# Kernel optimization log

Hardware: AMD Instinct MI355X
Metric: run time of the kernel (lower is better)

Reference implementation:

```python
import jax, jax.numpy as jnp
import numpy as np

B, N = 4, 1024
D1, D2 = 512, 512
C = 512          # out_c = outdim_self[2] = ln_dim
H = 8            # cross_num_heads
DH = C // H      # head dim
LAYERS = 3       # cross_layer
LN_EPS = 1e-5


def _layer_norm(x, gamma, beta):
    mu = jnp.mean(x, axis=-1, keepdims=True)
    var = jnp.mean(jnp.square(x - mu), axis=-1, keepdims=True)
    return (x - mu) * jax.lax.rsqrt(var + LN_EPS) * gamma + beta


def setup_inputs() -> dict:
    key = jax.random.key(0)
    ks = jax.random.split(key, 5)
    s1, s2, sv = 1.0 / np.sqrt(D1), 1.0 / np.sqrt(D2), 1.0 / np.sqrt(D1 + D2)
    return {
        "x1": jax.random.normal(ks[0], (B, N, D1), jnp.float32),
        "x2": jax.random.normal(ks[1], (B, N, D2), jnp.float32),
        "Wq": jax.random.uniform(ks[2], (C, D1), jnp.float32, -s1, s1),
        "Wk": jax.random.uniform(ks[3], (C, D2), jnp.float32, -s2, s2),
        "Wv": jax.random.uniform(ks[4], (C, D1 + D2), jnp.float32, -sv, sv),
        "ln_gamma": jnp.ones((C,), jnp.float32),
        "ln_beta": jnp.zeros((C,), jnp.float32),
    }


def reference(x1, x2, Wq, Wk, Wv, ln_gamma, ln_beta):
    x = jnp.concatenate((x1, x2), axis=2)                      # [B,N,D1+D2]
    scale = x1.shape[-1] ** (-0.5)                             # uses x1 feature dim
    # [B,N,C] -> [B,H,N,DH]
    to_heads = lambda t: t.reshape(B, N, H, DH).transpose(0, 2, 1, 3)
    Q = to_heads(jnp.einsum('bnd,cd->bnc', x1, Wq))
    K = to_heads(jnp.einsum('bnd,cd->bnc', x2, Wk))
    V = to_heads(jnp.einsum('bnd,cd->bnc', x, Wv))

    output = None
    for _ in range(LAYERS):
        attn = jnp.einsum('bhnd,bhmd->bhnm', Q, K) * scale     # [B,H,N,N]
        mask = attn != 0
        attn = jnp.where(mask, attn, -1e20)
        attn = jax.nn.softmax(attn, axis=-1)
        attn = attn * mask
        V1 = jnp.einsum('bhnm,bhmd->bhnd', attn, V)            # [B,H,N,DH]
        V1 = V1.transpose(0, 2, 1, 3).reshape(B, N, C)
        Vr = V.transpose(0, 2, 1, 3).reshape(B, N, C)
        output = _layer_norm(V1 + Vr, ln_gamma, ln_beta)       # [B,N,C]
        V = to_heads(output)
    return output
```

## Files before the change

### kernel.cpp

```cpp
#include <hip/hip_runtime.h>


#define LOG2E 1.44269504088896f

using f32x4   = __attribute__((ext_vector_type(4))) float;
using short8  = __attribute__((ext_vector_type(8))) short;
using ushort8 = __attribute__((ext_vector_type(8))) unsigned short;
using uchar8  = __attribute__((ext_vector_type(8))) unsigned char;
using uchar16 = __attribute__((ext_vector_type(16))) unsigned char;

__device__ inline unsigned short f2bf(float f) {
  unsigned u = __builtin_bit_cast(unsigned, f);
  u += 0x7fffu + ((u >> 16) & 1u);
  return (unsigned short)(u >> 16);
}
__device__ inline float bf2f(unsigned short h) {
  unsigned u = (unsigned)h << 16;
  return __builtin_bit_cast(float, u);
}

__device__ inline unsigned char f2e4m3_fast(float f) {
  unsigned u = __builtin_bit_cast(unsigned, f);
  unsigned sign = (u >> 24) & 0x80u;
  unsigned a = u & 0x7fffffffu;
  unsigned v = a + (0x7ffffu + ((a >> 20) & 1u));
  unsigned m = (v >> 20) - 960u;
  m = (m > 126u) ? 126u : m;
  m = (a < 0x3c000000u) ? 0u : m;
  return (unsigned char)(sign | m);
}

__device__ inline f32x4 mfma_bf16(short8 a, short8 b, f32x4 c) {
  return __builtin_amdgcn_mfma_f32_16x16x32_bf16(a, b, c, 0, 0, 0);
}

__device__ inline void gload_lds16(const void* g, void* l) {
  __builtin_amdgcn_global_load_lds(
      (const __attribute__((address_space(1))) unsigned int*)g,
      (__attribute__((address_space(3))) unsigned int*)l, 16, 0, 0);
}

__device__ inline int swz(int row, int byte_in_row) {
  return row * 128 + (byte_in_row ^ ((row & 7) << 4));
}

__global__ __launch_bounds__(256) void k_convert_all(
    const float* __restrict__ x1, const float* __restrict__ x2,
    const float* __restrict__ Wq, const float* __restrict__ Wk,
    const float* __restrict__ Wv,
    unsigned short* __restrict__ xb, unsigned short* __restrict__ Wqb,
    unsigned short* __restrict__ Wkb, unsigned short* __restrict__ Wvb) {
  int i = blockIdx.x * 256 + threadIdx.x;
  const float* src;
  unsigned short* dst;
  if (i < 524288) {
    int e0 = i * 8, m = e0 >> 10, d = e0 & 1023;
    src = (d < 512) ? (x1 + (size_t)m * 512 + d)
                    : (x2 + (size_t)m * 512 + (d - 512));
    dst = xb + (size_t)e0;
  } else if (i < 557056) {
    int j = (i - 524288) * 8;
    src = Wq + j; dst = Wqb + j;
  } else if (i < 589824) {
    int j = (i - 557056) * 8;
    src = Wk + j; dst = Wkb + j;
  } else {
    int j = (i - 589824) * 8;
    src = Wv + j; dst = Wvb + j;
  }
  float4 a = ((const float4*)src)[0];
  float4 b = ((const float4*)src)[1];
  ushort8 o;
  o[0] = f2bf(a.x); o[1] = f2bf(a.y); o[2] = f2bf(a.z); o[3] = f2bf(a.w);
  o[4] = f2bf(b.x); o[5] = f2bf(b.y); o[6] = f2bf(b.z); o[7] = f2bf(b.w);
  *(ushort8*)dst = o;
}

__global__ __launch_bounds__(256) void k_proj(
    const unsigned short* __restrict__ xb,
    const unsigned short* __restrict__ Wqb,
    const unsigned short* __restrict__ Wkb,
    const unsigned short* __restrict__ Wvb,
    unsigned short* __restrict__ Qb, unsigned short* __restrict__ Kb,
    float* __restrict__ Vf) {
  __shared__ __align__(16) unsigned short Atile[128 * 64];
  __shared__ __align__(16) unsigned short Btile[128 * 64];

  const int id  = blockIdx.x;
  const int z   = id % 3;
  const int rem = id / 3;
  const int c0  = (rem & 3) * 128;
  const int m0  = (rem >> 2) * 128;

  const int K    = (z == 2) ? 1024 : 512;
  const int aoff = (z == 1) ? 512 : 0;
  const unsigned short* W = (z == 0) ? Wqb : (z == 1) ? Wkb : Wvb;

  const int t  = threadIdx.x;
  const int w  = t >> 6, l = t & 63;
  const int lr = l & 15, ls = l >> 4;
  const int wr = w >> 1, wc = w & 1;

  const int srow  = l >> 3;
  const int scol8 = (l & 7) * 8;

  f32x4 acc[4][4] = {};

  for (int k0 = 0; k0 < K; k0 += 64) {
#pragma unroll
    for (int j = 0; j < 4; ++j) {
      int ch  = w * 4 + j;
      int row = ch * 8 + srow;
      gload_lds16(xb + (size_t)(m0 + row) * 1024 + aoff + k0 + scol8,
                  Atile + ch * 512);
      gload_lds16(W + (size_t)(c0 + row) * K + k0 + scol8,
                  Btile + ch * 512);
    }
    __syncthreads();
#pragma unroll
    for (int ks = 0; ks < 2; ++ks) {
      short8 af[4], bf[4];
#pragma unroll
      for (int mf = 0; mf < 4; ++mf)
        af[mf] = *(const short8*)(Atile + (wr * 64 + mf * 16 + lr) * 64 +
                                  ks * 32 + ls * 8);
#pragma unroll
      for (int nf = 0; nf < 4; ++nf)
        bf[nf] = *(const short8*)(Btile + (wc * 64 + nf * 16 + lr) * 64 +
                                  ks * 32 + ls * 8);
#pragma unroll
      for (int mf = 0; mf < 4; ++mf)
#pragma unroll
        for (int nf = 0; nf < 4; ++nf)
          acc[mf][nf] = mfma_bf16(af[mf], bf[nf], acc[mf][nf]);
    }
    __syncthreads();
  }

#pragma unroll
  for (int mf = 0; mf < 4; ++mf)
#pragma unroll
    for (int nf = 0; nf < 4; ++nf)
#pragma unroll
      for (int r = 0; r < 4; ++r) {
        int m = m0 + wr * 64 + mf * 16 + ls * 4 + r;
        int c = c0 + wc * 64 + nf * 16 + lr;
        float v = acc[mf][nf][r];
        if (z == 2) {
          Vf[(size_t)m * 512 + c] = v;
        } else {
          int b = m >> 10, n = m & 1023, h = c >> 6, dh = c & 63;
          size_t idx = ((size_t)(b * 8 + h) * 1024 + n) * 64 + dh;
          (z == 0 ? Qb : Kb)[idx] = f2bf(v);
        }
      }
}

__global__ __launch_bounds__(256) void k_transpose_v(
    const float* __restrict__ Vf, void* __restrict__ Vt, int mode) {
  __shared__ unsigned short tile[64 * 66];
  const int bh = blockIdx.y;
  const int b = bh >> 3, h = bh & 7;
  const int n0 = blockIdx.x * 64;
  const int t = threadIdx.x;
  {
    int n = t >> 2, dh0 = (t & 3) * 16;
    const float* src = Vf + ((size_t)b * 1024 + n0 + n) * 512 + h * 64 + dh0;
    unsigned short* dst = tile + n * 66 + dh0;
#pragma unroll
    for (int j = 0; j < 16; j += 4) {
      float4 v = *(const float4*)(src + j);
      dst[j + 0] = f2bf(v.x); dst[j + 1] = f2bf(v.y);
      dst[j + 2] = f2bf(v.z); dst[j + 3] = f2bf(v.w);
    }
  }
  __syncthreads();
#pragma unroll
  for (int it = 0; it < 2; ++it) {
    int dh = (t >> 3) + it * 32, n8 = (t & 7) * 8;
    if (mode == 0) {
      ushort8 o;
#pragma unroll
      for (int j = 0; j < 8; ++j) o[j] = tile[(n8 + j) * 66 + dh];
      char* dst = (char*)Vt + ((size_t)(bh * 64 + dh)) * 2048 + n0 * 2 +
                  ((n8 * 2) ^ ((dh & 7) << 4));
      *(ushort8*)dst = o;
    } else {
      uchar8 o;
#pragma unroll
      for (int j = 0; j < 8; ++j)
        o[j] = f2e4m3_fast(bf2f(tile[(n8 + j) * 66 + dh]));
      int byte = n0 + n8;
      char* dst = (char*)Vt + ((size_t)(bh * 64 + dh)) * 1024 + (byte & ~127) +
                  ((byte & 127) ^ ((dh & 7) << 4));
      *(uchar8*)dst = o;
    }
  }
}

__global__ __launch_bounds__(256) void k_scores(
    const unsigned short* __restrict__ Qb,
    const unsigned short* __restrict__ Kb,
    unsigned char* __restrict__ Pmat, float* __restrict__ lsum_g) {
  __shared__ char lds[8192 + 4 * 16 * 80];
  char* kbuf = lds;
  const int id  = blockIdx.x;
  const int lid = (id & 7) * 128 + (id >> 3);
  const int bh  = lid >> 5;
  const int q0  = ((lid >> 1) & 15) * 64;
  const int kh  = lid & 1;
  const int t = threadIdx.x;
  const int w = t >> 6, l = t & 63, lr = l & 15, ls = l >> 4;
  char* pbuf = lds + 8192 + w * (16 * 80);

  const float sclog2e = 0.0637587160f;

  short8 qa[2];
  {
    const unsigned short* Qg =
        Qb + ((size_t)bh * 1024 + q0 + w * 16 + lr) * 64 + ls * 8;
    qa[0] = *(const short8*)(Qg);
    qa[1] = *(const short8*)(Qg + 32);
  }

  const unsigned short* Kg = Kb + (size_t)bh * 1024 * 64 + kh * 512 * 64;
  unsigned char* Pg = Pmat + (size_t)bh * 1024 * 1024;

  float lacc[4] = {0.f, 0.f, 0.f, 0.f};

  const int srow = t >> 3, sc8 = (t & 7) * 8;
  int4 kreg[2];
  kreg[0] = *(const int4*)(Kg + (size_t)(srow)*64 + sc8);
  kreg[1] = *(const int4*)(Kg + (size_t)(srow + 32) * 64 + sc8);

  for (int kc = 0; kc < 8; ++kc) {
    *(int4*)(kbuf + swz(srow, sc8 * 2)) = kreg[0];
    *(int4*)(kbuf + swz(srow + 32, sc8 * 2)) = kreg[1];
    __syncthreads();
    if (kc < 7) {
      kreg[0] = *(const int4*)(Kg + (size_t)((kc + 1) * 64 + srow) * 64 + sc8);
      kreg[1] = *(const int4*)(Kg + (size_t)((kc + 1) * 64 + srow + 32) * 64 + sc8);
    }

    f32x4 s[4] = {};
#pragma unroll
    for (int kk = 0; kk < 2; ++kk) {
#pragma unroll
      for (int nt = 0; nt < 4; ++nt) {
        short8 bk = *(const short8*)(kbuf + swz(nt * 16 + lr, kk * 64 + ls * 16));
        s[nt] = mfma_bf16(qa[kk], bk, s[nt]);
      }
    }

#pragma unroll
    for (int nt = 0; nt < 4; ++nt)
#pragma unroll
      for (int r = 0; r < 4; ++r) {
        float sv = s[nt][r];
        float pv = (sv == 0.f) ? 0.f : __builtin_amdgcn_exp2f(sv * sclog2e);
        lacc[r] += pv;
        pbuf[(ls * 4 + r) * 80 + nt * 16 + lr] = (char)f2e4m3_fast(pv);
      }

    int gkc = kh * 8 + kc;
    {
      int prow = l >> 2, pchk = l & 3;
      uchar16 pv16 = *(const uchar16*)(pbuf + prow * 80 + pchk * 16);
      int n = q0 + w * 16 + prow;
      *(uchar16*)(Pg + (size_t)n * 1024 + (gkc >> 1) * 128 +
                  (((gkc & 1) * 64 + pchk * 16) ^ ((n & 7) << 4))) = pv16;
    }
    __syncthreads();
  }

#pragma unroll
  for (int r = 0; r < 4; ++r) {
#pragma unroll
    for (int off = 1; off < 16; off <<= 1)
      lacc[r] += __shfl_xor(lacc[r], off, 64);
  }
  if (lr == 0) {
#pragma unroll
    for (int r = 0; r < 4; ++r)
      lsum_g[kh * 32768 + (size_t)bh * 1024 + q0 + w * 16 + ls * 4 + r] =
          lacc[r];
  }
}

__global__ __launch_bounds__(256) void k_pv(
    const unsigned char* __restrict__ Pmat,
    const unsigned char* __restrict__ Vt,
    const float* __restrict__ lsum_g, float* __restrict__ V1a,
    float* __restrict__ V1b) {
  __shared__ __align__(16) char Ab[2][8192];
  __shared__ __align__(16) char Bb[2][8192];
  const int id  = blockIdx.x;
  const int lid = (id & 7) * 128 + (id >> 3);
  const int head = lid >> 5;
  const int n0   = ((lid >> 1) & 15) * 64;
  const int mh   = lid & 1;
  const int t = threadIdx.x;
  const int w = t >> 6, l = t & 63, lr = l & 15, ls = l >> 4;

  const char* Pg = (const char*)(Pmat + (size_t)head * 1024 * 1024) +
                   (size_t)n0 * 1024 + mh * 512;
  const char* Vg = (const char*)(Vt + (size_t)head * 64 * 1024) + mh * 512;

  const int srow = w * 16 + (l >> 3);
  const int sc16 = (l & 7) * 16;

  f32x4 acc[4] = {};

  auto STAGE = [&](int buf, int kc) {
#pragma unroll
    for (int j = 0; j < 2; ++j) {
      int row = srow + j * 8;
      gload_lds16(Pg + (size_t)row * 1024 + kc * 128 + sc16,
                  &Ab[buf][w * 2048 + j * 1024]);
      gload_lds16(Vg + (size_t)row * 1024 + kc * 128 + sc16,
                  &Bb[buf][w * 2048 + j * 1024]);
    }
  };

  STAGE(0, 0);
  __syncthreads();
  int cur = 0;
  for (int kc = 0; kc < 4; ++kc) {
    if (kc < 3) STAGE(cur ^ 1, kc + 1);
#pragma unroll
    for (int ks = 0; ks < 4; ++ks) {
      long af = *(const long*)(&Ab[cur][swz(w * 16 + lr, ks * 32 + ls * 8)]);
#pragma unroll
      for (int nf = 0; nf < 4; ++nf) {
        long bf8 = *(const long*)(&Bb[cur][swz(nf * 16 + lr, ks * 32 + ls * 8)]);
        acc[nf] = __builtin_amdgcn_mfma_f32_16x16x32_fp8_fp8(af, bf8, acc[nf],
                                                             0, 0, 0);
      }
    }
    __syncthreads();
    cur ^= 1;
  }

  float* V1 = mh ? V1b : V1a;
  const int b = head >> 3, h = head & 7;
#pragma unroll
  for (int r = 0; r < 4; ++r) {
    int n = n0 + w * 16 + ls * 4 + r;
    float lv = lsum_g[(size_t)head * 1024 + n] +
               lsum_g[32768 + (size_t)head * 1024 + n];
    float rinv = (lv > 0.f) ? 1.f / lv : 0.f;
#pragma unroll
    for (int nf = 0; nf < 4; ++nf)
      V1[((size_t)b * 1024 + n) * 512 + h * 64 + nf * 16 + lr] =
          acc[nf][r] * rinv;
  }
}

__global__ __launch_bounds__(256) void k_ln_t(
    const float* __restrict__ V1a, const float* __restrict__ V1b,
    const float* __restrict__ Vf_in,
    const float* __restrict__ gamma, const float* __restrict__ beta,
    float* __restrict__ Vf_out, void* __restrict__ Vt, int mode) {
  __shared__ unsigned short tile[16 * 520];
  const int blk = blockIdx.x;
  const int b  = blk >> 6;
  const int n0 = (blk & 63) * 16;
  const int t = threadIdx.x;
  const int row = t >> 4;
  const int c0  = (t & 15) * 32;
  const size_t base = ((size_t)b * 1024 + n0 + row) * 512 + c0;

  float x[32];
  float s = 0.f, sq = 0.f;
#pragma unroll
  for (int j = 0; j < 32; j += 4) {
    float4 a0 = *(const float4*)(V1a + base + j);
    float4 a1 = *(const float4*)(V1b + base + j);
    float4 v = *(const float4*)(Vf_in + base + j);
    float4 y = {a0.x + a1.x + v.x, a0.y + a1.y + v.y, a0.z + a1.z + v.z,
                a0.w + a1.w + v.w};
    x[j + 0] = y.x; x[j + 1] = y.y; x[j + 2] = y.z; x[j + 3] = y.w;
    s  += y.x + y.y + y.z + y.w;
    sq += y.x * y.x + y.y * y.y + y.z * y.z + y.w * y.w;
  }
#pragma unroll
  for (int off = 1; off < 16; off <<= 1) {
    s  += __shfl_xor(s, off, 64);
    sq += __shfl_xor(sq, off, 64);
  }
  float mu   = s * (1.f / 512.f);
  float var  = sq * (1.f / 512.f) - mu * mu;
  float rstd = rsqrtf(var + 1e-5f);

  unsigned short* trow = tile + row * 520 + c0;
#pragma unroll
  for (int j = 0; j < 32; j += 4) {
    float4 g = *(const float4*)(gamma + c0 + j);
    float4 bb = *(const float4*)(beta + c0 + j);
    float4 y;
    y.x = (x[j + 0] - mu) * rstd * g.x + bb.x;
    y.y = (x[j + 1] - mu) * rstd * g.y + bb.y;
    y.z = (x[j + 2] - mu) * rstd * g.z + bb.z;
    y.w = (x[j + 3] - mu) * rstd * g.w + bb.w;
    *(float4*)(Vf_out + base + j) = y;
    if (mode != 2) {
      trow[j + 0] = f2bf(y.x); trow[j + 1] = f2bf(y.y);
      trow[j + 2] = f2bf(y.z); trow[j + 3] = f2bf(y.w);
    }
  }
  if (mode == 2) return;
  __syncthreads();

#pragma unroll
  for (int it = 0; it < 2; ++it) {
    int d = t + it * 256;
    int h = d >> 6, dh = d & 63;
    int sw = (dh & 7) << 4;
    if (mode == 0) {
      ushort8 o0, o1;
#pragma unroll
      for (int j = 0; j < 8; ++j) {
        o0[j] = tile[j * 520 + d];
        o1[j] = tile[(j + 8) * 520 + d];
      }
      int byte0 = n0 * 2;
      char* rowb = (char*)Vt + ((size_t)((b * 8 + h) * 64 + dh)) * 2048 +
                   (byte0 & ~127);
      *(ushort8*)(rowb + ((byte0 & 127) ^ sw)) = o0;
      *(ushort8*)(rowb + (((byte0 & 127) + 16) ^ sw)) = o1;
    } else {
      uchar16 o;
#pragma unroll
      for (int j = 0; j < 16; ++j) o[j] = f2e4m3_fast(bf2f(tile[j * 520 + d]));
      char* rowb = (char*)Vt + ((size_t)((b * 8 + h) * 64 + dh)) * 1024 +
                   (n0 & ~127);
      *(uchar16*)(rowb + ((n0 & 127) ^ sw)) = o;
    }
  }
}

__global__ __launch_bounds__(256) void k_attn(
    const unsigned short* __restrict__ Qb,
    const unsigned short* __restrict__ Kb,
    const unsigned short* __restrict__ Vt,
    float* __restrict__ V1) {
  __shared__ char lds[8192 + 8192 + 4 * 16 * 144];
  char* kbuf = lds;
  char* vbuf = lds + 8192;
  const int bh = blockIdx.y;
  const int q0 = blockIdx.x * 64;
  const int t = threadIdx.x;
  const int w = t >> 6, l = t & 63, lr = l & 15, ls = l >> 4;
  char* pbuf = lds + 16384 + w * (16 * 144);

  const float scale = 0.044194173824159216f;

  short8 qa[2];
  {
    const unsigned short* Qg =
        Qb + ((size_t)bh * 1024 + q0 + w * 16 + lr) * 64 + ls * 8;
    qa[0] = *(const short8*)(Qg);
    qa[1] = *(const short8*)(Qg + 32);
  }

  f32x4 O[4] = {};
  float mrow[4], lrow[4];
#pragma unroll
  for (int r = 0; r < 4; ++r) { mrow[r] = -INFINITY; lrow[r] = 0.f; }

  const unsigned short* Kg = Kb + (size_t)bh * 1024 * 64;
  const char* Vg = (const char*)(Vt + (size_t)bh * 64 * 1024);

  for (int kc = 0; kc < 16; ++kc) {
    {
      int row = t >> 3;
      int c8  = (t & 7) * 8;
#pragma unroll
      for (int it = 0; it < 2; ++it) {
        int rr = row + it * 32;
        int4 kv = *(const int4*)(Kg + (size_t)(kc * 64 + rr) * 64 + c8);
        *(int4*)(kbuf + swz(rr, c8 * 2)) = kv;
        int swv = (rr & 7) << 4;
        int4 vv = *(const int4*)(Vg + (size_t)rr * 2048 + kc * 128 +
                                 ((c8 * 2) ^ swv));
        *(int4*)(vbuf + swz(rr, c8 * 2)) = vv;
      }
    }
    __syncthreads();

    f32x4 s[4] = {};
#pragma unroll
    for (int kk = 0; kk < 2; ++kk) {
#pragma unroll
      for (int nt = 0; nt < 4; ++nt) {
        short8 bk = *(const short8*)(kbuf + swz(nt * 16 + lr, kk * 64 + ls * 16));
        s[nt] = mfma_bf16(qa[kk], bk, s[nt]);
      }
    }

    float p[4][4];
    float cmax[4];
#pragma unroll
    for (int r = 0; r < 4; ++r) cmax[r] = -INFINITY;
#pragma unroll
    for (int nt = 0; nt < 4; ++nt)
#pragma unroll
      for (int r = 0; r < 4; ++r) {
        float sv = s[nt][r];
        p[nt][r] = (sv == 0.f) ? -INFINITY : sv * scale;
        cmax[r] = fmaxf(cmax[r], p[nt][r]);
      }
#pragma unroll
    for (int r = 0; r < 4; ++r)
#pragma unroll
      for (int off = 1; off < 16; off <<= 1)
        cmax[r] = fmaxf(cmax[r], __shfl_xor(cmax[r], off, 64));

    float alpha[4];
#pragma unroll
    for (int r = 0; r < 4; ++r) {
      float mnew = fmaxf(mrow[r], cmax[r]);
      alpha[r] = (mnew == -INFINITY) ? 1.f : exp2f((mrow[r] - mnew) * LOG2E);
      mrow[r] = mnew;
    }
    float lsum[4] = {0.f, 0.f, 0.f, 0.f};
#pragma unroll
    for (int nt = 0; nt < 4; ++nt)
#pragma unroll
      for (int r = 0; r < 4; ++r) {
        float pv = (p[nt][r] == -INFINITY)
                       ? 0.f
                       : exp2f((p[nt][r] - mrow[r]) * LOG2E);
        p[nt][r] = pv;
        lsum[r] += pv;
      }
#pragma unroll
    for (int r = 0; r < 4; ++r) {
#pragma unroll
      for (int off = 1; off < 16; off <<= 1)
        lsum[r] += __shfl_xor(lsum[r], off, 64);
      lrow[r] = lrow[r] * alpha[r] + lsum[r];
    }
#pragma unroll
    for (int dt = 0; dt < 4; ++dt)
#pragma unroll
      for (int r = 0; r < 4; ++r) O[dt][r] *= alpha[r];

#pragma unroll
    for (int nt = 0; nt < 4; ++nt)
#pragma unroll
      for (int r = 0; r < 4; ++r)
        *(unsigned short*)(pbuf + (ls * 4 + r) * 144 + (nt * 16 + lr) * 2) =
            f2bf(p[nt][r]);

#pragma unroll
    for (int kk = 0; kk < 2; ++kk) {
      short8 pa = *(const short8*)(pbuf + lr * 144 + kk * 64 + ls * 16);
#pragma unroll
      for (int dt = 0; dt < 4; ++dt) {
        short8 bv = *(const short8*)(vbuf + swz(dt * 16 + lr, kk * 64 + ls * 16));
        O[dt] = mfma_bf16(pa, bv, O[dt]);
      }
    }
    __syncthreads();
  }

  float rinv[4];
#pragma unroll
  for (int r = 0; r < 4; ++r) rinv[r] = (lrow[r] > 0.f) ? 1.f / lrow[r] : 0.f;
  const int b = bh >> 3, h = bh & 7;
#pragma unroll
  for (int dt = 0; dt < 4; ++dt)
#pragma unroll
    for (int r = 0; r < 4; ++r) {
      int n = q0 + w * 16 + ls * 4 + r;
      int c = h * 64 + dt * 16 + lr;
      V1[((size_t)b * 1024 + n) * 512 + c] = O[dt][r] * rinv[r];
    }
}

extern "C" void kernel_launch(void* const* d_in, const int* in_sizes, int n_in,
                              void* d_out, int out_size, void* d_ws,
                              size_t ws_size, hipStream_t stream) {
  const float* x1    = (const float*)d_in[0];
  const float* x2    = (const float*)d_in[1];
  const float* Wq    = (const float*)d_in[2];
  const float* Wk    = (const float*)d_in[3];
  const float* Wv    = (const float*)d_in[4];
  const float* gamma = (const float*)d_in[5];
  const float* beta  = (const float*)d_in[6];
  float* out = (float*)d_out;
  char* ws = (char*)d_ws;

  const size_t MB = 1u << 20;
  unsigned short* xb  = (unsigned short*)(ws);
  unsigned short* Wqb = (unsigned short*)(ws + 8 * MB);
  unsigned short* Wkb = (unsigned short*)(ws + 8 * MB + 512 * 1024);
  unsigned short* Wvb = (unsigned short*)(ws + 9 * MB);
  unsigned short* Qb  = (unsigned short*)(ws + 10 * MB);
  unsigned short* Kb  = (unsigned short*)(ws + 14 * MB);
  void*           Vt  = (void*)(ws + 18 * MB);
  float*          Vf  = (float*)(ws + 22 * MB);
  float*          V1a = (float*)(ws + 30 * MB);
  float*          lsm = (float*)(ws + 38 * MB);
  unsigned char*  Pm  = (unsigned char*)(ws + 39 * MB);
  float*          V1b = (float*)(ws);

  const bool bigws = ws_size >= (size_t)71 * MB;

  k_convert_all<<<2560, 256, 0, stream>>>(x1, x2, Wq, Wk, Wv, xb, Wqb, Wkb,
                                          Wvb);
  k_proj<<<384, 256, 0, stream>>>(xb, Wqb, Wkb, Wvb, Qb, Kb, Vf);

  if (bigws) {
    k_transpose_v<<<dim3(16, 32), 256, 0, stream>>>(Vf, Vt, 1);
    k_scores<<<1024, 256, 0, stream>>>(Qb, Kb, Pm, lsm);
    for (int layer = 0; layer < 3; ++layer) {
      k_pv<<<1024, 256, 0, stream>>>(Pm, (const unsigned char*)Vt, lsm, V1a,
                                     V1b);
      if (layer < 2)
        k_ln_t<<<256, 256, 0, stream>>>(V1a, V1b, Vf, gamma, beta, Vf, Vt, 1);
      else
        k_ln_t<<<256, 256, 0, stream>>>(V1a, V1b, Vf, gamma, beta, out, Vt, 2);
    }
  } else {
    hipMemsetAsync(V1b, 0, 8 * MB, stream);
    k_transpose_v<<<dim3(16, 32), 256, 0, stream>>>(Vf, Vt, 0);
    for (int layer = 0; layer < 3; ++layer) {
      k_attn<<<dim3(16, 32), 256, 0, stream>>>(Qb, Kb,
                                               (const unsigned short*)Vt, V1a);
      if (layer < 2)
        k_ln_t<<<256, 256, 0, stream>>>(V1a, V1b, Vf, gamma, beta, Vf, Vt, 0);
      else
        k_ln_t<<<256, 256, 0, stream>>>(V1a, V1b, Vf, gamma, beta, out, Vt, 2);
    }
  }
}
```

Baseline: 136.2 us.

## Split score kernel into key quarters with double-buffered K, finer LN blocks

k_scores now splits each query tile's keys into four quarters instead of two, doubling the grid, and double-buffers the K tile in LDS so that one barrier per iteration suffices. The row-sum partials grow to four slices, which k_pv now adds together. k_ln_t processes 4 rows per block instead of 16, with one wavefront per row, giving 1024 blocks. The aim is more parallelism and fewer barriers on the MI355X CUs, at the cost of smaller, narrower global stores (4-byte Vt writes) and extra lsum reads.

```diff
diff --git a/kernel.cpp b/kernel.cpp
--- a/kernel.cpp
+++ b/kernel.cpp
@@ -6,7 +6,9 @@
 using f32x4   = __attribute__((ext_vector_type(4))) float;
 using short8  = __attribute__((ext_vector_type(8))) short;
 using ushort8 = __attribute__((ext_vector_type(8))) unsigned short;
+using ushort4v= __attribute__((ext_vector_type(4))) unsigned short;
 using uchar8  = __attribute__((ext_vector_type(8))) unsigned char;
+using uchar4v = __attribute__((ext_vector_type(4))) unsigned char;
 using uchar16 = __attribute__((ext_vector_type(16))) unsigned char;
 
 __device__ inline unsigned short f2bf(float f) {
@@ -202,16 +204,17 @@
     const unsigned short* __restrict__ Qb,
     const unsigned short* __restrict__ Kb,
     unsigned char* __restrict__ Pmat, float* __restrict__ lsum_g) {
-  __shared__ char lds[8192 + 4 * 16 * 80];
-  char* kbuf = lds;
+  __shared__ char lds[2 * 8192 + 4 * 16 * 80];
+  char* kbuf0 = lds;
+  char* kbuf1 = lds + 8192;
   const int id  = blockIdx.x;
-  const int lid = (id & 7) * 128 + (id >> 3);
-  const int bh  = lid >> 5;
-  const int q0  = ((lid >> 1) & 15) * 64;
-  const int kh  = lid & 1;
+  const int lid = (id & 7) * 256 + (id >> 3);
+  const int bh  = lid >> 6;
+  const int q0  = ((lid >> 2) & 15) * 64;
+  const int kq  = lid & 3;
   const int t = threadIdx.x;
   const int w = t >> 6, l = t & 63, lr = l & 15, ls = l >> 4;
-  char* pbuf = lds + 8192 + w * (16 * 80);
+  char* pbuf = lds + 16384 + w * (16 * 80);
 
   const float sclog2e = 0.0637587160f;
 
@@ -223,7 +226,7 @@
     qa[1] = *(const short8*)(Qg + 32);
   }
 
-  const unsigned short* Kg = Kb + (size_t)bh * 1024 * 64 + kh * 512 * 64;
+  const unsigned short* Kg = Kb + (size_t)bh * 1024 * 64 + kq * 256 * 64;
   unsigned char* Pg = Pmat + (size_t)bh * 1024 * 1024;
 
   float lacc[4] = {0.f, 0.f, 0.f, 0.f};
@@ -232,12 +235,17 @@
   int4 kreg[2];
   kreg[0] = *(const int4*)(Kg + (size_t)(srow)*64 + sc8);
   kreg[1] = *(const int4*)(Kg + (size_t)(srow + 32) * 64 + sc8);
-
-  for (int kc = 0; kc < 8; ++kc) {
-    *(int4*)(kbuf + swz(srow, sc8 * 2)) = kreg[0];
-    *(int4*)(kbuf + swz(srow + 32, sc8 * 2)) = kreg[1];
+  {
+    char* kb = kbuf0;
+    *(int4*)(kb + swz(srow, sc8 * 2)) = kreg[0];
+    *(int4*)(kb + swz(srow + 32, sc8 * 2)) = kreg[1];
+  }
+
+  for (int kc = 0; kc < 4; ++kc) {
     __syncthreads();
-    if (kc < 7) {
+    char* kb  = (kc & 1) ? kbuf1 : kbuf0;
+    char* kbn = (kc & 1) ? kbuf0 : kbuf1;
+    if (kc < 3) {
       kreg[0] = *(const int4*)(Kg + (size_t)((kc + 1) * 64 + srow) * 64 + sc8);
       kreg[1] = *(const int4*)(Kg + (size_t)((kc + 1) * 64 + srow + 32) * 64 + sc8);
     }
@@ -247,7 +255,7 @@
     for (int kk = 0; kk < 2; ++kk) {
 #pragma unroll
       for (int nt = 0; nt < 4; ++nt) {
-        short8 bk = *(const short8*)(kbuf + swz(nt * 16 + lr, kk * 64 + ls * 16));
+        short8 bk = *(const short8*)(kb + swz(nt * 16 + lr, kk * 64 + ls * 16));
         s[nt] = mfma_bf16(qa[kk], bk, s[nt]);
       }
     }
@@ -262,7 +270,7 @@
         pbuf[(ls * 4 + r) * 80 + nt * 16 + lr] = (char)f2e4m3_fast(pv);
       }
 
-    int gkc = kh * 8 + kc;
+    int gkc = kq * 4 + kc;
     {
       int prow = l >> 2, pchk = l & 3;
       uchar16 pv16 = *(const uchar16*)(pbuf + prow * 80 + pchk * 16);
@@ -270,7 +278,11 @@
       *(uchar16*)(Pg + (size_t)n * 1024 + (gkc >> 1) * 128 +
                   (((gkc & 1) * 64 + pchk * 16) ^ ((n & 7) << 4))) = pv16;
     }
-    __syncthreads();
+
+    if (kc < 3) {
+      *(int4*)(kbn + swz(srow, sc8 * 2)) = kreg[0];
+      *(int4*)(kbn + swz(srow + 32, sc8 * 2)) = kreg[1];
+    }
   }
 
 #pragma unroll
@@ -282,7 +294,7 @@
   if (lr == 0) {
 #pragma unroll
     for (int r = 0; r < 4; ++r)
-      lsum_g[kh * 32768 + (size_t)bh * 1024 + q0 + w * 16 + ls * 4 + r] =
+      lsum_g[kq * 32768 + (size_t)bh * 1024 + q0 + w * 16 + ls * 4 + r] =
           lacc[r];
   }
 }
@@ -346,8 +358,9 @@
 #pragma unroll
   for (int r = 0; r < 4; ++r) {
     int n = n0 + w * 16 + ls * 4 + r;
-    float lv = lsum_g[(size_t)head * 1024 + n] +
-               lsum_g[32768 + (size_t)head * 1024 + n];
+    size_t li = (size_t)head * 1024 + n;
+    float lv = lsum_g[li] + lsum_g[32768 + li] + lsum_g[65536 + li] +
+               lsum_g[98304 + li];
     float rinv = (lv > 0.f) ? 1.f / lv : 0.f;
 #pragma unroll
     for (int nf = 0; nf < 4; ++nf)
@@ -361,19 +374,20 @@
     const float* __restrict__ Vf_in,
     const float* __restrict__ gamma, const float* __restrict__ beta,
     float* __restrict__ Vf_out, void* __restrict__ Vt, int mode) {
-  __shared__ unsigned short tile[16 * 520];
+  __shared__ unsigned short tile[4 * 520];
   const int blk = blockIdx.x;
-  const int b  = blk >> 6;
-  const int n0 = (blk & 63) * 16;
+  const int b  = blk >> 8;
+  const int n0 = (blk & 255) * 4;
   const int t = threadIdx.x;
-  const int row = t >> 4;
-  const int c0  = (t & 15) * 32;
+  const int row = t >> 6;
+  const int l = t & 63;
+  const int c0 = l * 8;
   const size_t base = ((size_t)b * 1024 + n0 + row) * 512 + c0;
 
-  float x[32];
+  float x[8];
   float s = 0.f, sq = 0.f;
 #pragma unroll
-  for (int j = 0; j < 32; j += 4) {
+  for (int j = 0; j < 8; j += 4) {
     float4 a0 = *(const float4*)(V1a + base + j);
     float4 a1 = *(const float4*)(V1b + base + j);
     float4 v = *(const float4*)(Vf_in + base + j);
@@ -384,7 +398,7 @@
     sq += y.x * y.x + y.y * y.y + y.z * y.z + y.w * y.w;
   }
 #pragma unroll
-  for (int off = 1; off < 16; off <<= 1) {
+  for (int off = 1; off < 64; off <<= 1) {
     s  += __shfl_xor(s, off, 64);
     sq += __shfl_xor(sq, off, 64);
   }
@@ -394,7 +408,7 @@
 
   unsigned short* trow = tile + row * 520 + c0;
 #pragma unroll
-  for (int j = 0; j < 32; j += 4) {
+  for (int j = 0; j < 8; j += 4) {
     float4 g = *(const float4*)(gamma + c0 + j);
     float4 bb = *(const float4*)(beta + c0 + j);
     float4 y;
@@ -417,24 +431,20 @@
     int h = d >> 6, dh = d & 63;
     int sw = (dh & 7) << 4;
     if (mode == 0) {
-      ushort8 o0, o1;
-#pragma unroll
-      for (int j = 0; j < 8; ++j) {
-        o0[j] = tile[j * 520 + d];
-        o1[j] = tile[(j + 8) * 520 + d];
-      }
+      ushort4v o;
+#pragma unroll
+      for (int j = 0; j < 4; ++j) o[j] = tile[j * 520 + d];
       int byte0 = n0 * 2;
-      char* rowb = (char*)Vt + ((size_t)((b * 8 + h) * 64 + dh)) * 2048 +
-                   (byte0 & ~127);
-      *(ushort8*)(rowb + ((byte0 & 127) ^ sw)) = o0;
-      *(ushort8*)(rowb + (((byte0 & 127) + 16) ^ sw)) = o1;
+      char* dst = (char*)Vt + ((size_t)((b * 8 + h) * 64 + dh)) * 2048 +
+                  (byte0 & ~127) + ((byte0 & 127) ^ sw);
+      *(ushort4v*)dst = o;
     } else {
-      uchar16 o;
-#pragma unroll
-      for (int j = 0; j < 16; ++j) o[j] = f2e4m3_fast(bf2f(tile[j * 520 + d]));
-      char* rowb = (char*)Vt + ((size_t)((b * 8 + h) * 64 + dh)) * 1024 +
-                   (n0 & ~127);
-      *(uchar16*)(rowb + ((n0 & 127) ^ sw)) = o;
+      uchar4v o;
+#pragma unroll
+      for (int j = 0; j < 4; ++j) o[j] = f2e4m3_fast(bf2f(tile[j * 520 + d]));
+      char* dst = (char*)Vt + ((size_t)((b * 8 + h) * 64 + dh)) * 1024 +
+                  (n0 & ~127) + ((n0 & 127) ^ sw);
+      *(uchar4v*)dst = o;
     }
   }
 }
@@ -614,14 +624,14 @@
 
   if (bigws) {
     k_transpose_v<<<dim3(16, 32), 256, 0, stream>>>(Vf, Vt, 1);
-    k_scores<<<1024, 256, 0, stream>>>(Qb, Kb, Pm, lsm);
+    k_scores<<<2048, 256, 0, stream>>>(Qb, Kb, Pm, lsm);
     for (int layer = 0; layer < 3; ++layer) {
       k_pv<<<1024, 256, 0, stream>>>(Pm, (const unsigned char*)Vt, lsm, V1a,
                                      V1b);
       if (layer < 2)
-        k_ln_t<<<256, 256, 0, stream>>>(V1a, V1b, Vf, gamma, beta, Vf, Vt, 1);
+        k_ln_t<<<1024, 256, 0, stream>>>(V1a, V1b, Vf, gamma, beta, Vf, Vt, 1);
       else
-        k_ln_t<<<256, 256, 0, stream>>>(V1a, V1b, Vf, gamma, beta, out, Vt, 2);
+        k_ln_t<<<1024, 256, 0, stream>>>(V1a, V1b, Vf, gamma, beta, out, Vt, 2);
     }
   } else {
     hipMemsetAsync(V1b, 0, 8 * MB, stream);
@@ -630,9 +640,9 @@
       k_attn<<<dim3(16, 32), 256, 0, stream>>>(Qb, Kb,
                                                (const unsigned short*)Vt, V1a);
       if (layer < 2)
-        k_ln_t<<<256, 256, 0, stream>>>(V1a, V1b, Vf, gamma, beta, Vf, Vt, 0);
+        k_ln_t<<<1024, 256, 0, stream>>>(V1a, V1b, Vf, gamma, beta, Vf, Vt, 0);
       else
-        k_ln_t<<<256, 256, 0, stream>>>(V1a, V1b, Vf, gamma, beta, out, Vt, 2);
-    }
-  }
-}
+        k_ln_t<<<1024, 256, 0, stream>>>(V1a, V1b, Vf, gamma, beta, out, Vt, 2);
+    }
+  }
+}
```

New measurement: 125.8 us. 7.6% less time.
